# Kernel tuning notes

Hardware: AMD Instinct MI355X
Metric: run time of the kernel (lower is better)

The kernel has to match this reference:

```python
import jax, jax.numpy as jnp
import numpy as np

B, T, C, H = 4, 2048, 1024, 16
D = C // H  # head dim = 64


def setup_inputs() -> dict:
    key = jax.random.key(0)
    ks = jax.random.split(key, 5)
    s = 0.02
    return {
        "x": jax.random.normal(ks[0], (B, T, C), dtype=jnp.float32),
        "W_attn": jax.random.normal(ks[1], (C, 3 * C), dtype=jnp.float32) * s,
        "b_attn": jnp.zeros((3 * C,), dtype=jnp.float32),
        "W_proj": jax.random.normal(ks[2], (C, C), dtype=jnp.float32) * s,
        "b_proj": jnp.zeros((C,), dtype=jnp.float32),
    }


def reference(x, W_attn, b_attn, W_proj, b_proj):
    # qkv projection: [B,T,3C]
    qkv = x @ W_attn + b_attn
    q, k, v = jnp.split(qkv, 3, axis=-1)
    # [B,T,C] -> [B,H,T,D]
    def heads(t):
        return t.reshape(B, T, H, D).transpose(0, 2, 1, 3)
    q, k, v = heads(q), heads(k), heads(v)
    # scaled scores with causal mask, materialized [B,H,T,T] as in original
    att = jnp.einsum('bhqd,bhkd->bhqk', q, k) * (1.0 / np.sqrt(D))
    causal = jnp.tril(jnp.ones((T, T), dtype=bool))
    att = jnp.where(causal[None, None], att, -jnp.inf)
    att = jax.nn.softmax(att, axis=-1)
    y = jnp.einsum('bhqk,bhkd->bhqd', att, v)  # [B,H,T,D]
    y = y.transpose(0, 2, 1, 3).reshape(B, T, C)
    y = y @ W_proj + b_proj
    # original also returns present=(k,v); it is a pure pass-through cache
    return y
```

## Files before the change

kernel.cpp:

```cpp
#include <hip/hip_runtime.h>


typedef unsigned short u16;
typedef unsigned int u32;
typedef __attribute__((ext_vector_type(8))) unsigned short u16x8;
typedef __attribute__((ext_vector_type(4))) unsigned short u16x4;
typedef __attribute__((ext_vector_type(8))) short short8;
typedef __attribute__((ext_vector_type(4))) float f32x4;

__device__ inline u16 f2bf(float f) {
  unsigned u = __float_as_uint(f);
  u = (u + 0x7FFF + ((u >> 16) & 1)) >> 16;
  return (u16)u;
}

__device__ inline f32x4 mfma16(short8 a, short8 b, f32x4 c) {
  return __builtin_amdgcn_mfma_f32_16x16x32_bf16(a, b, c, 0, 0, 0);
}

__global__ __launch_bounds__(256) void k_cvt(const float* __restrict__ in,
                                             u16* __restrict__ out) {
  int i = (blockIdx.x * 256 + threadIdx.x) * 4;
  float4 v = *(const float4*)(in + i);
  u16x4 o = {f2bf(v.x), f2bf(v.y), f2bf(v.z), f2bf(v.w)};
  *(u16x4*)(out + i) = o;
}

__global__ __launch_bounds__(256) void k_tw(const float* __restrict__ in,
                                            u16* __restrict__ outT, int R, int Cc) {
  __shared__ u16 t[64][65];
  int c0 = blockIdx.x * 64, r0 = blockIdx.y * 64;
  int a = threadIdx.x & 63, w = threadIdx.x >> 6;
#pragma unroll
  for (int j = 0; j < 16; ++j) {
    int r = w + j * 4;
    t[r][a] = f2bf(in[(size_t)(r0 + r) * Cc + c0 + a]);
  }
  __syncthreads();
#pragma unroll
  for (int j = 0; j < 16; ++j) {
    int c = w + j * 4;
    outT[(size_t)(c0 + c) * R + r0 + a] = t[a][c];
  }
}

__global__ __launch_bounds__(256) void k_tv(const u16* __restrict__ qkv,
                                            u16* __restrict__ vt) {
  __shared__ u16 t[64][65];
  int t0 = blockIdx.x * 64, h = blockIdx.y, b = blockIdx.z;
  int a = threadIdx.x & 63, w = threadIdx.x >> 6;
#pragma unroll
  for (int j = 0; j < 16; ++j) {
    int tr = w + j * 4;
    t[tr][a] = qkv[(size_t)(b * 2048 + t0 + tr) * 3072 + 2048 + h * 64 + a];
  }
  __syncthreads();
#pragma unroll
  for (int j = 0; j < 16; ++j) {
    int d = w + j * 4;
    vt[((size_t)((b * 16 + h) * 64 + d)) * 2048 + t0 + a] = t[a][d];
  }
}

template <int OUTBF, int QSCALE>
__global__ __launch_bounds__(256) void gemm_bt(const u16* __restrict__ A,
                                               const u16* __restrict__ Bt,
                                               const float* __restrict__ bias,
                                               u16* __restrict__ outb,
                                               float* __restrict__ outf,
                                               int M, int N, int K) {
  __shared__ u16 As[128 * 64];
  __shared__ u16 Bs[128 * 64];
  const int nx = gridDim.x, ny = gridDim.y;
  int id0 = blockIdx.x + blockIdx.y * nx;
  int nwg = nx * ny;
  int q8 = nwg >> 3, x8 = id0 & 7, c8 = id0 >> 3;
  int id = x8 * q8 + c8;
  int gs = 8 * ny, grp = id / gs, rem = id % gs;
  const int m0 = (grp * 8 + (rem & 7)) * 128, n0 = (rem >> 3) * 128;

  const int tid = threadIdx.x, wave = tid >> 6, lane = tid & 63;
  const int quad = lane >> 4, l16 = lane & 15;
  const int wm = (wave & 1) * 64, wn = (wave >> 1) * 64;
  const int lrow = lane >> 3;
  const int lch = lane & 7;
  const int slot = lch ^ lrow;
  const u16* sA[4];
  const u16* sB[4];
  int offA[4], offB[4];
#pragma unroll
  for (int j = 0; j < 4; ++j) {
    int r = wave * 32 + j * 8;
    sA[j] = A + (size_t)(m0 + r + lrow) * K + lch * 8;
    sB[j] = Bt + (size_t)(n0 + r + lrow) * K + lch * 8;
    offA[j] = (r + lrow) * 64 + slot * 8;
    offB[j] = offA[j];
  }
  u16x8 ra[4], rb[4];
#pragma unroll
  for (int j = 0; j < 4; ++j) {
    ra[j] = *(const u16x8*)(sA[j]);
    rb[j] = *(const u16x8*)(sB[j]);
  }
  f32x4 acc[4][4] = {};
  for (int kt = 0; kt < K; kt += 64) {
    __syncthreads();
#pragma unroll
    for (int j = 0; j < 4; ++j) {
      *(u16x8*)&As[offA[j]] = ra[j];
      *(u16x8*)&Bs[offB[j]] = rb[j];
    }
    __syncthreads();
    if (kt + 64 < K) {
#pragma unroll
      for (int j = 0; j < 4; ++j) {
        ra[j] = *(const u16x8*)(sA[j] + kt + 64);
        rb[j] = *(const u16x8*)(sB[j] + kt + 64);
      }
    }
    const int sl = l16 & 7;
#pragma unroll
    for (int ks = 0; ks < 2; ++ks) {
      short8 af[4], bf[4];
#pragma unroll
      for (int mt = 0; mt < 4; ++mt)
        af[mt] = *(const short8*)(As + (wm + mt * 16 + l16) * 64 +
                                  ((ks * 4 + quad) ^ sl) * 8);
#pragma unroll
      for (int nt = 0; nt < 4; ++nt)
        bf[nt] = *(const short8*)(Bs + (wn + nt * 16 + l16) * 64 +
                                  ((ks * 4 + quad) ^ sl) * 8);
#pragma unroll
      for (int mt = 0; mt < 4; ++mt)
#pragma unroll
        for (int nt = 0; nt < 4; ++nt)
          acc[mt][nt] = mfma16(af[mt], bf[nt], acc[mt][nt]);
    }
  }
#pragma unroll
  for (int nt = 0; nt < 4; ++nt) {
    int col = n0 + wn + nt * 16 + l16;
    float bv = bias[col];
#pragma unroll
    for (int mt = 0; mt < 4; ++mt) {
      int rowb = m0 + wm + mt * 16 + quad * 4;
#pragma unroll
      for (int r = 0; r < 4; ++r) {
        float v = acc[mt][nt][r] + bv;
        if (QSCALE && col < 1024) v *= 0.18033688f;
        if (OUTBF)
          outb[(size_t)(rowb + r) * N + col] = f2bf(v);
        else
          outf[(size_t)(rowb + r) * N + col] = v;
      }
    }
  }
}

#define ATP 72
__global__ __launch_bounds__(256) void attn(const u16* __restrict__ qkv,
                                            const u16* __restrict__ vt,
                                            u16* __restrict__ y) {
  __shared__ u16 shm[256 * ATP];
  u16* Qs = shm;
  u16* Ks = shm + 128 * ATP;
  u16* Vs = shm + 192 * ATP;
  const int p = blockIdx.x, h = blockIdx.y, b = blockIdx.z;
  const int tid = threadIdx.x, wave = tid >> 6, lane = tid & 63;
  const int quad = lane >> 4, l16 = lane & 15;
  const u16* Qg = qkv + (size_t)b * 2048 * 3072 + h * 64;
  const u16* Kg = Qg + 1024;
  const u16* Vtg = vt + (size_t)(b * 16 + h) * 64 * 2048;
  const int srow0 = tid >> 3, scol0 = (tid & 7) * 8;
  u16* Pw0 = Qs + (wave * 16) * ATP;
  u16* Pw1 = Qs + (64 + wave * 16) * ATP;
  short8 ones_f;
#pragma unroll
  for (int j = 0; j < 8; ++j) ones_f[j] = 0x3F80;

  for (int half = 0; half < 2; ++half) {
    const int qb = half ? (15 - p) : p;
    const int q0 = qb * 128;
    const int nkt = 2 * qb + 2;
    const u16* kp0 = Kg + (size_t)srow0 * 3072 + scol0;
    const u16* kp1 = kp0 + 32 * 3072;
    const u16* vp0 = Vtg + (size_t)srow0 * 2048 + scol0;
    const u16* vp1 = vp0 + 32 * 2048;
    u16x8 qr0 = *(const u16x8*)(Qg + (size_t)(q0 + srow0) * 3072 + scol0);
    u16x8 qr1 = *(const u16x8*)(Qg + (size_t)(q0 + srow0 + 32) * 3072 + scol0);
    u16x8 qr2 = *(const u16x8*)(Qg + (size_t)(q0 + srow0 + 64) * 3072 + scol0);
    u16x8 qr3 = *(const u16x8*)(Qg + (size_t)(q0 + srow0 + 96) * 3072 + scol0);
    u16x8 kreg0 = *(const u16x8*)kp0, kreg1 = *(const u16x8*)kp1;
    u16x8 vreg0 = *(const u16x8*)vp0, vreg1 = *(const u16x8*)vp1;
    __syncthreads();
    *(u16x8*)&Qs[(size_t)srow0 * ATP + scol0] = qr0;
    *(u16x8*)&Qs[(size_t)(srow0 + 32) * ATP + scol0] = qr1;
    *(u16x8*)&Qs[(size_t)(srow0 + 64) * ATP + scol0] = qr2;
    *(u16x8*)&Qs[(size_t)(srow0 + 96) * ATP + scol0] = qr3;
    *(u16x8*)&Ks[(size_t)srow0 * ATP + scol0] = kreg0;
    *(u16x8*)&Ks[(size_t)(srow0 + 32) * ATP + scol0] = kreg1;
    *(u16x8*)&Vs[(size_t)srow0 * ATP + scol0] = vreg0;
    *(u16x8*)&Vs[(size_t)(srow0 + 32) * ATP + scol0] = vreg1;
    __syncthreads();
    short8 qf0a = *(const short8*)&Qs[(wave * 16 + l16) * ATP + quad * 8];
    short8 qf1a = *(const short8*)&Qs[(wave * 16 + l16) * ATP + 32 + quad * 8];
    short8 qf0b = *(const short8*)&Qs[(64 + wave * 16 + l16) * ATP + quad * 8];
    short8 qf1b = *(const short8*)&Qs[(64 + wave * 16 + l16) * ATP + 32 + quad * 8];

    f32x4 lacc0 = {}, lacc1 = {};
    f32x4 o0[4] = {}, o1[4] = {};

    auto tile = [&](int kt, int g0mode, bool g1mask) {
      if (kt > 0) {
        __syncthreads();
        *(u16x8*)&Ks[(size_t)srow0 * ATP + scol0] = kreg0;
        *(u16x8*)&Ks[(size_t)(srow0 + 32) * ATP + scol0] = kreg1;
        *(u16x8*)&Vs[(size_t)srow0 * ATP + scol0] = vreg0;
        *(u16x8*)&Vs[(size_t)(srow0 + 32) * ATP + scol0] = vreg1;
        __syncthreads();
      }
      if (kt + 1 < nkt) {
        kreg0 = *(const u16x8*)(kp0 += 64 * 3072);
        kreg1 = *(const u16x8*)(kp1 += 64 * 3072);
        vreg0 = *(const u16x8*)(vp0 += 64);
        vreg1 = *(const u16x8*)(vp1 += 64);
      }

      f32x4 s0[4] = {}, s1[4] = {};
#pragma unroll
      for (int mt = 0; mt < 4; ++mt) {
        short8 kf0 = *(const short8*)&Ks[(mt * 16 + l16) * ATP + quad * 8];
        short8 kf1 = *(const short8*)&Ks[(mt * 16 + l16) * ATP + 32 + quad * 8];
        if (g0mode < 2) {
          s0[mt] = mfma16(kf0, qf0a, s0[mt]);
          s0[mt] = mfma16(kf1, qf1a, s0[mt]);
        }
        s1[mt] = mfma16(kf0, qf0b, s1[mt]);
        s1[mt] = mfma16(kf1, qf1b, s1[mt]);
      }

      if (g0mode < 2) {
        const int qrow = q0 + wave * 16 + l16;
#pragma unroll
        for (int mt = 0; mt < 4; ++mt) {
          float pe[4];
#pragma unroll
          for (int r = 0; r < 4; ++r) {
            float pv = __builtin_amdgcn_exp2f(s0[mt][r]);
            if (g0mode == 1) {
              int kcol = kt * 64 + mt * 16 + quad * 4 + r;
              if (kcol > qrow) pv = 0.f;
            }
            pe[r] = pv;
          }
          u32 lo = __builtin_amdgcn_perm(__float_as_uint(pe[1]),
                                         __float_as_uint(pe[0]), 0x07060302u);
          u32 hi = __builtin_amdgcn_perm(__float_as_uint(pe[3]),
                                         __float_as_uint(pe[2]), 0x07060302u);
          uint2 pk = {lo, hi};
          *(uint2*)&Pw0[l16 * ATP + mt * 16 + quad * 4] = pk;
        }
      }
      {
        const int qrow = q0 + 64 + wave * 16 + l16;
#pragma unroll
        for (int mt = 0; mt < 4; ++mt) {
          float pe[4];
#pragma unroll
          for (int r = 0; r < 4; ++r) {
            float pv = __builtin_amdgcn_exp2f(s1[mt][r]);
            if (g1mask) {
              int kcol = kt * 64 + mt * 16 + quad * 4 + r;
              if (kcol > qrow) pv = 0.f;
            }
            pe[r] = pv;
          }
          u32 lo = __builtin_amdgcn_perm(__float_as_uint(pe[1]),
                                         __float_as_uint(pe[0]), 0x07060302u);
          u32 hi = __builtin_amdgcn_perm(__float_as_uint(pe[3]),
                                         __float_as_uint(pe[2]), 0x07060302u);
          uint2 pk = {lo, hi};
          *(uint2*)&Pw1[l16 * ATP + mt * 16 + quad * 4] = pk;
        }
      }

#pragma unroll
      for (int ks = 0; ks < 2; ++ks) {
        short8 pf0, pf1;
        if (g0mode < 2) {
          pf0 = *(const short8*)&Pw0[l16 * ATP + ks * 32 + quad * 8];
          lacc0 = mfma16(pf0, ones_f, lacc0);
        }
        pf1 = *(const short8*)&Pw1[l16 * ATP + ks * 32 + quad * 8];
        lacc1 = mfma16(pf1, ones_f, lacc1);
#pragma unroll
        for (int dt = 0; dt < 4; ++dt) {
          short8 vf = *(const short8*)&Vs[(dt * 16 + l16) * ATP + ks * 32 + quad * 8];
          if (g0mode < 2) o0[dt] = mfma16(pf0, vf, o0[dt]);
          o1[dt] = mfma16(pf1, vf, o1[dt]);
        }
      }
    };

    for (int kt = 0; kt < nkt - 2; ++kt) tile(kt, 0, false);
    tile(nkt - 2, 1, false);
    tile(nkt - 1, 2, true);

    size_t rb0 = (size_t)b * 2048 + q0 + wave * 16 + quad * 4;
#pragma unroll
    for (int r = 0; r < 4; ++r) {
      float inv = 1.f / lacc0[r];
#pragma unroll
      for (int dt = 0; dt < 4; ++dt)
        y[(rb0 + r) * 1024 + h * 64 + dt * 16 + l16] = f2bf(o0[dt][r] * inv);
    }
    size_t rb1 = rb0 + 64;
#pragma unroll
    for (int r = 0; r < 4; ++r) {
      float inv = 1.f / lacc1[r];
#pragma unroll
      for (int dt = 0; dt < 4; ++dt)
        y[(rb1 + r) * 1024 + h * 64 + dt * 16 + l16] = f2bf(o1[dt][r] * inv);
    }
  }
}

extern "C" void kernel_launch(void* const* d_in, const int* in_sizes, int n_in,
                              void* d_out, int out_size, void* d_ws, size_t ws_size,
                              hipStream_t stream) {
  const float* x = (const float*)d_in[0];
  const float* W_attn = (const float*)d_in[1];
  const float* b_attn = (const float*)d_in[2];
  const float* W_proj = (const float*)d_in[3];
  const float* b_proj = (const float*)d_in[4];
  float* out = (float*)d_out;
  char* ws = (char*)d_ws;
  u16* xb  = (u16*)(ws);
  u16* wta = (u16*)(ws + 16777216);
  u16* wtp = (u16*)(ws + 23068672);
  u16* qkv = (u16*)(ws + 25165824);
  u16* vt  = (u16*)(ws + 75497472);
  u16* y   = (u16*)(ws + 92274688);

  k_cvt<<<dim3(8192), 256, 0, stream>>>(x, xb);
  k_tw<<<dim3(48, 16), 256, 0, stream>>>(W_attn, wta, 1024, 3072);
  k_tw<<<dim3(16, 16), 256, 0, stream>>>(W_proj, wtp, 1024, 1024);
  gemm_bt<1, 1><<<dim3(64, 24), 256, 0, stream>>>(xb, wta, b_attn, qkv, nullptr, 8192, 3072, 1024);
  k_tv<<<dim3(32, 16, 4), 256, 0, stream>>>(qkv, vt);
  attn<<<dim3(8, 16, 4), 256, 0, stream>>>(qkv, vt, y);
  gemm_bt<0, 0><<<dim3(64, 8), 256, 0, stream>>>(y, wtp, b_proj, nullptr, out, 8192, 1024, 1024);
}
```

Measured before the change: 250.9 us.

## Enlarge attention query tile to 256 rows and reorder causal blocks per batch

```diff
diff --git a/kernel.cpp b/kernel.cpp
--- a/kernel.cpp
+++ b/kernel.cpp
@@ -158,96 +158,104 @@
 }
 
 #define ATP 72
-__global__ __launch_bounds__(256) void attn(const u16* __restrict__ qkv,
-                                            const u16* __restrict__ vt,
-                                            u16* __restrict__ y) {
-  __shared__ u16 shm[256 * ATP];
+__global__ __launch_bounds__(256, 2) void attn(const u16* __restrict__ qkv,
+                                               const u16* __restrict__ vt,
+                                               u16* __restrict__ y) {
+  __shared__ u16 shm[384 * ATP];
   u16* Qs = shm;
-  u16* Ks = shm + 128 * ATP;
-  u16* Vs = shm + 192 * ATP;
-  const int p = blockIdx.x, h = blockIdx.y, b = blockIdx.z;
+  u16* Ks = shm + 256 * ATP;
+  u16* Vs = shm + 320 * ATP;
+  const int xx = blockIdx.x, h = blockIdx.y, b = blockIdx.z;
+  const int qb = (b < 2) ? (7 - xx) : xx;
+  const int q0 = qb * 256;
+  const int nkt = 4 * qb + 4;
   const int tid = threadIdx.x, wave = tid >> 6, lane = tid & 63;
   const int quad = lane >> 4, l16 = lane & 15;
   const u16* Qg = qkv + (size_t)b * 2048 * 3072 + h * 64;
   const u16* Kg = Qg + 1024;
   const u16* Vtg = vt + (size_t)(b * 16 + h) * 64 * 2048;
   const int srow0 = tid >> 3, scol0 = (tid & 7) * 8;
-  u16* Pw0 = Qs + (wave * 16) * ATP;
-  u16* Pw1 = Qs + (64 + wave * 16) * ATP;
   short8 ones_f;
 #pragma unroll
   for (int j = 0; j < 8; ++j) ones_f[j] = 0x3F80;
 
-  for (int half = 0; half < 2; ++half) {
-    const int qb = half ? (15 - p) : p;
-    const int q0 = qb * 128;
-    const int nkt = 2 * qb + 2;
-    const u16* kp0 = Kg + (size_t)srow0 * 3072 + scol0;
-    const u16* kp1 = kp0 + 32 * 3072;
-    const u16* vp0 = Vtg + (size_t)srow0 * 2048 + scol0;
-    const u16* vp1 = vp0 + 32 * 2048;
-    u16x8 qr0 = *(const u16x8*)(Qg + (size_t)(q0 + srow0) * 3072 + scol0);
-    u16x8 qr1 = *(const u16x8*)(Qg + (size_t)(q0 + srow0 + 32) * 3072 + scol0);
-    u16x8 qr2 = *(const u16x8*)(Qg + (size_t)(q0 + srow0 + 64) * 3072 + scol0);
-    u16x8 qr3 = *(const u16x8*)(Qg + (size_t)(q0 + srow0 + 96) * 3072 + scol0);
-    u16x8 kreg0 = *(const u16x8*)kp0, kreg1 = *(const u16x8*)kp1;
-    u16x8 vreg0 = *(const u16x8*)vp0, vreg1 = *(const u16x8*)vp1;
-    __syncthreads();
-    *(u16x8*)&Qs[(size_t)srow0 * ATP + scol0] = qr0;
-    *(u16x8*)&Qs[(size_t)(srow0 + 32) * ATP + scol0] = qr1;
-    *(u16x8*)&Qs[(size_t)(srow0 + 64) * ATP + scol0] = qr2;
-    *(u16x8*)&Qs[(size_t)(srow0 + 96) * ATP + scol0] = qr3;
-    *(u16x8*)&Ks[(size_t)srow0 * ATP + scol0] = kreg0;
-    *(u16x8*)&Ks[(size_t)(srow0 + 32) * ATP + scol0] = kreg1;
-    *(u16x8*)&Vs[(size_t)srow0 * ATP + scol0] = vreg0;
-    *(u16x8*)&Vs[(size_t)(srow0 + 32) * ATP + scol0] = vreg1;
-    __syncthreads();
-    short8 qf0a = *(const short8*)&Qs[(wave * 16 + l16) * ATP + quad * 8];
-    short8 qf1a = *(const short8*)&Qs[(wave * 16 + l16) * ATP + 32 + quad * 8];
-    short8 qf0b = *(const short8*)&Qs[(64 + wave * 16 + l16) * ATP + quad * 8];
-    short8 qf1b = *(const short8*)&Qs[(64 + wave * 16 + l16) * ATP + 32 + quad * 8];
-
-    f32x4 lacc0 = {}, lacc1 = {};
-    f32x4 o0[4] = {}, o1[4] = {};
-
-    auto tile = [&](int kt, int g0mode, bool g1mask) {
-      if (kt > 0) {
-        __syncthreads();
-        *(u16x8*)&Ks[(size_t)srow0 * ATP + scol0] = kreg0;
-        *(u16x8*)&Ks[(size_t)(srow0 + 32) * ATP + scol0] = kreg1;
-        *(u16x8*)&Vs[(size_t)srow0 * ATP + scol0] = vreg0;
-        *(u16x8*)&Vs[(size_t)(srow0 + 32) * ATP + scol0] = vreg1;
-        __syncthreads();
-      }
-      if (kt + 1 < nkt) {
-        kreg0 = *(const u16x8*)(kp0 += 64 * 3072);
-        kreg1 = *(const u16x8*)(kp1 += 64 * 3072);
-        vreg0 = *(const u16x8*)(vp0 += 64);
-        vreg1 = *(const u16x8*)(vp1 += 64);
-      }
-
-      f32x4 s0[4] = {}, s1[4] = {};
+  const u16* kp0 = Kg + (size_t)srow0 * 3072 + scol0;
+  const u16* kp1 = kp0 + 32 * 3072;
+  const u16* vp0 = Vtg + (size_t)srow0 * 2048 + scol0;
+  const u16* vp1 = vp0 + 32 * 2048;
+  u16x8 qr[8];
+#pragma unroll
+  for (int j = 0; j < 8; ++j)
+    qr[j] = *(const u16x8*)(Qg + (size_t)(q0 + srow0 + 32 * j) * 3072 + scol0);
+  u16x8 kreg0 = *(const u16x8*)kp0, kreg1 = *(const u16x8*)kp1;
+  u16x8 vreg0 = *(const u16x8*)vp0, vreg1 = *(const u16x8*)vp1;
+#pragma unroll
+  for (int j = 0; j < 8; ++j)
+    *(u16x8*)&Qs[(size_t)(srow0 + 32 * j) * ATP + scol0] = qr[j];
+  *(u16x8*)&Ks[(size_t)srow0 * ATP + scol0] = kreg0;
+  *(u16x8*)&Ks[(size_t)(srow0 + 32) * ATP + scol0] = kreg1;
+  *(u16x8*)&Vs[(size_t)srow0 * ATP + scol0] = vreg0;
+  *(u16x8*)&Vs[(size_t)(srow0 + 32) * ATP + scol0] = vreg1;
+  __syncthreads();
+  short8 qf[4][2];
+#pragma unroll
+  for (int g = 0; g < 4; ++g) {
+    qf[g][0] = *(const short8*)&Qs[(g * 64 + wave * 16 + l16) * ATP + quad * 8];
+    qf[g][1] = *(const short8*)&Qs[(g * 64 + wave * 16 + l16) * ATP + 32 + quad * 8];
+  }
+
+  f32x4 lacc[4] = {};
+  f32x4 o[4][4] = {};
+
+  for (int kt = 0; kt < nkt; ++kt) {
+    if (kt > 0) {
+      __syncthreads();
+      *(u16x8*)&Ks[(size_t)srow0 * ATP + scol0] = kreg0;
+      *(u16x8*)&Ks[(size_t)(srow0 + 32) * ATP + scol0] = kreg1;
+      *(u16x8*)&Vs[(size_t)srow0 * ATP + scol0] = vreg0;
+      *(u16x8*)&Vs[(size_t)(srow0 + 32) * ATP + scol0] = vreg1;
+      __syncthreads();
+    }
+    if (kt + 1 < nkt) {
+      kreg0 = *(const u16x8*)(kp0 += 64 * 3072);
+      kreg1 = *(const u16x8*)(kp1 += 64 * 3072);
+      vreg0 = *(const u16x8*)(vp0 += 64);
+      vreg1 = *(const u16x8*)(vp1 += 64);
+    }
+    const int c = kt - (nkt - 4);
+
+#pragma unroll
+    for (int j = 0; j < 2; ++j) {
+      const int gA = 2 * j, gB = gA + 1;
+      if (c > gB) continue;
+      const int mA = (c < gA) ? 0 : ((c == gA) ? 1 : 2);
+      const bool bmask = (c == gB);
+
+      f32x4 sA[4] = {}, sB[4] = {};
 #pragma unroll
       for (int mt = 0; mt < 4; ++mt) {
         short8 kf0 = *(const short8*)&Ks[(mt * 16 + l16) * ATP + quad * 8];
         short8 kf1 = *(const short8*)&Ks[(mt * 16 + l16) * ATP + 32 + quad * 8];
-        if (g0mode < 2) {
-          s0[mt] = mfma16(kf0, qf0a, s0[mt]);
-          s0[mt] = mfma16(kf1, qf1a, s0[mt]);
-        }
-        s1[mt] = mfma16(kf0, qf0b, s1[mt]);
-        s1[mt] = mfma16(kf1, qf1b, s1[mt]);
-      }
-
-      if (g0mode < 2) {
-        const int qrow = q0 + wave * 16 + l16;
+        if (mA < 2) {
+          sA[mt] = mfma16(kf0, qf[gA][0], sA[mt]);
+          sA[mt] = mfma16(kf1, qf[gA][1], sA[mt]);
+        }
+        sB[mt] = mfma16(kf0, qf[gB][0], sB[mt]);
+        sB[mt] = mfma16(kf1, qf[gB][1], sB[mt]);
+      }
+
+      u16* PwA = Qs + (gA * 64 + wave * 16) * ATP;
+      u16* PwB = Qs + (gB * 64 + wave * 16) * ATP;
+      if (mA < 2) {
+        const int qrow = q0 + gA * 64 + wave * 16 + l16;
+        const bool masked = (mA == 1);
 #pragma unroll
         for (int mt = 0; mt < 4; ++mt) {
           float pe[4];
 #pragma unroll
           for (int r = 0; r < 4; ++r) {
-            float pv = __builtin_amdgcn_exp2f(s0[mt][r]);
-            if (g0mode == 1) {
+            float pv = __builtin_amdgcn_exp2f(sA[mt][r]);
+            if (masked) {
               int kcol = kt * 64 + mt * 16 + quad * 4 + r;
               if (kcol > qrow) pv = 0.f;
             }
@@ -258,18 +266,18 @@
           u32 hi = __builtin_amdgcn_perm(__float_as_uint(pe[3]),
                                          __float_as_uint(pe[2]), 0x07060302u);
           uint2 pk = {lo, hi};
-          *(uint2*)&Pw0[l16 * ATP + mt * 16 + quad * 4] = pk;
+          *(uint2*)&PwA[l16 * ATP + mt * 16 + quad * 4] = pk;
         }
       }
       {
-        const int qrow = q0 + 64 + wave * 16 + l16;
+        const int qrow = q0 + gB * 64 + wave * 16 + l16;
 #pragma unroll
         for (int mt = 0; mt < 4; ++mt) {
           float pe[4];
 #pragma unroll
           for (int r = 0; r < 4; ++r) {
-            float pv = __builtin_amdgcn_exp2f(s1[mt][r]);
-            if (g1mask) {
+            float pv = __builtin_amdgcn_exp2f(sB[mt][r]);
+            if (bmask) {
               int kcol = kt * 64 + mt * 16 + quad * 4 + r;
               if (kcol > qrow) pv = 0.f;
             }
@@ -280,47 +288,38 @@
           u32 hi = __builtin_amdgcn_perm(__float_as_uint(pe[3]),
                                          __float_as_uint(pe[2]), 0x07060302u);
           uint2 pk = {lo, hi};
-          *(uint2*)&Pw1[l16 * ATP + mt * 16 + quad * 4] = pk;
+          *(uint2*)&PwB[l16 * ATP + mt * 16 + quad * 4] = pk;
         }
       }
 
 #pragma unroll
       for (int ks = 0; ks < 2; ++ks) {
-        short8 pf0, pf1;
-        if (g0mode < 2) {
-          pf0 = *(const short8*)&Pw0[l16 * ATP + ks * 32 + quad * 8];
-          lacc0 = mfma16(pf0, ones_f, lacc0);
-        }
-        pf1 = *(const short8*)&Pw1[l16 * ATP + ks * 32 + quad * 8];
-        lacc1 = mfma16(pf1, ones_f, lacc1);
+        short8 pfA, pfB;
+        if (mA < 2) {
+          pfA = *(const short8*)&PwA[l16 * ATP + ks * 32 + quad * 8];
+          lacc[gA] = mfma16(pfA, ones_f, lacc[gA]);
+        }
+        pfB = *(const short8*)&PwB[l16 * ATP + ks * 32 + quad * 8];
+        lacc[gB] = mfma16(pfB, ones_f, lacc[gB]);
 #pragma unroll
         for (int dt = 0; dt < 4; ++dt) {
           short8 vf = *(const short8*)&Vs[(dt * 16 + l16) * ATP + ks * 32 + quad * 8];
-          if (g0mode < 2) o0[dt] = mfma16(pf0, vf, o0[dt]);
-          o1[dt] = mfma16(pf1, vf, o1[dt]);
-        }
-      }
-    };
-
-    for (int kt = 0; kt < nkt - 2; ++kt) tile(kt, 0, false);
-    tile(nkt - 2, 1, false);
-    tile(nkt - 1, 2, true);
-
-    size_t rb0 = (size_t)b * 2048 + q0 + wave * 16 + quad * 4;
+          if (mA < 2) o[gA][dt] = mfma16(pfA, vf, o[gA][dt]);
+          o[gB][dt] = mfma16(pfB, vf, o[gB][dt]);
+        }
+      }
+    }
+  }
+
+#pragma unroll
+  for (int g = 0; g < 4; ++g) {
+    size_t rb = (size_t)b * 2048 + q0 + g * 64 + wave * 16 + quad * 4;
 #pragma unroll
     for (int r = 0; r < 4; ++r) {
-      float inv = 1.f / lacc0[r];
+      float inv = 1.f / lacc[g][r];
 #pragma unroll
       for (int dt = 0; dt < 4; ++dt)
-        y[(rb0 + r) * 1024 + h * 64 + dt * 16 + l16] = f2bf(o0[dt][r] * inv);
-    }
-    size_t rb1 = rb0 + 64;
-#pragma unroll
-    for (int r = 0; r < 4; ++r) {
-      float inv = 1.f / lacc1[r];
-#pragma unroll
-      for (int dt = 0; dt < 4; ++dt)
-        y[(rb1 + r) * 1024 + h * 64 + dt * 16 + l16] = f2bf(o1[dt][r] * inv);
+        y[(rb + r) * 1024 + h * 64 + dt * 16 + l16] = f2bf(o[g][dt][r] * inv);
     }
   }
 }
```

After: 270.9 us. +7.9%, slower.
